# Optimization experiments

Measured on AMD Instinct MI355X. Metric: run time of the kernel, lower is better.

## Reference

```python
import jax, jax.numpy as jnp
import numpy as np


def setup_inputs() -> dict:
    key = jax.random.key(0)
    k1, k2, k3, k4 = jax.random.split(key, 4)
    B, G, C, T = 4, 40, 13, 1024
    return {
        "x": jax.random.normal(k1, (B, G, C, T), dtype=jnp.float32),
        "query_w": jax.random.normal(k2, (C, C), dtype=jnp.float32),
        "key_w": jax.random.normal(k3, (C, C), dtype=jnp.float32),
        "value_w": jax.random.normal(k4, (C, C), dtype=jnp.float32),
    }


def reference(x, query_w, key_w, value_w):
    # x: [B, 40, 13, T] real -> rfft over time -> [B, 40, 13, F] complex
    x_fft = jnp.fft.rfft(x, axis=-1)
    cdt = x_fft.dtype
    wq = query_w.astype(cdt)  # [13,13] complex (zero imag), shared across the 40 groups
    wk = key_w.astype(cdt)
    wv = value_w.astype(cdt)
    xt = jnp.swapaxes(x_fft, -1, -2)  # [B, 40, F, 13]
    q = xt @ wq                       # [B, 40, F, 13]
    k = xt @ wk
    v = xt @ wv
    scores = jnp.abs(q @ jnp.swapaxes(k, -1, -2))     # [B, 40, F, F] real
    attn = jax.nn.softmax(scores, axis=-1).astype(cdt)
    out = (attn @ v)                                   # [B, 40, F, 13]
    out = jnp.swapaxes(out, -1, -2)                    # [B, 40, 13, F]
    return jnp.fft.irfft(out, axis=-1)                 # [B, 40, 13, 2*(F-1)]
```

## Files before the change

kernel.cpp:

```cpp
#include <hip/hip_runtime.h>
#include <math.h>

#define BDIM 4
#define GDIM 40
#define CDIM 13
#define TDIM 1024
#define FDIM 513
#define BG   (BDIM*GDIM)
#define NROW (BG*FDIM)
#define NCHUNK 9
#define TK 64
#define QW 64

typedef _Float16 half4 __attribute__((ext_vector_type(4)));
typedef _Float16 half8 __attribute__((ext_vector_type(8)));
typedef float    f32x4 __attribute__((ext_vector_type(4)));

#define MFMA16(a, b, c) __builtin_amdgcn_mfma_f32_16x16x16f16((a), (b), (c), 0, 0, 0)

__device__ __forceinline__ unsigned bitrev10(unsigned x) { return __brev(x) >> 22; }

#define IDX(i) ((i) + ((i) >> 5))

__global__ __launch_bounds__(256) void fft_fwd2(const float* __restrict__ x,
                                                float2* __restrict__ xf) {
    __shared__ float re[1056], im[1056];
    const int s2 = blockIdx.x;
    const int sigA = 2 * s2, sigB = sigA + 1;
    const float* x1 = x + (size_t)sigA * TDIM;
    const float* x2 = x1 + TDIM;
    for (int t = threadIdx.x; t < 1024; t += 256) {
        unsigned r = bitrev10(t);
        re[IDX(r)] = x1[t];
        im[IDX(r)] = x2[t];
    }
    __syncthreads();
    for (int s = 0; s < 10; s += 2) {
        const int h   = 1 << s;
        const int g   = threadIdx.x;
        const int grp = g >> s;
        const int pos = g & (h - 1);
        const int i0  = (grp << (s + 2)) + pos;
        const int j0 = IDX(i0), j1 = IDX(i0 + h), j2 = IDX(i0 + 2 * h), j3 = IDX(i0 + 3 * h);
        float w1s, w1c, w2s, w2c;
        __sincosf(-(float)M_PI * (float)pos / (float)h, &w1s, &w1c);
        __sincosf(-(float)M_PI * (float)pos / (float)(2 * h), &w2s, &w2c);
        float ar = re[j0], ai = im[j0], br = re[j1], bi = im[j1];
        float cr = re[j2], ci = im[j2], dr = re[j3], di = im[j3];
        float t1;
        t1 = w1c * br - w1s * bi; bi = w1c * bi + w1s * br; br = t1;
        t1 = w1c * dr - w1s * di; di = w1c * di + w1s * dr; dr = t1;
        float e0r = ar + br, e0i = ai + bi, e1r = ar - br, e1i = ai - bi;
        float f0r = cr + dr, f0i = ci + di, f1r = cr - dr, f1i = ci - di;
        t1 = w2c * f0r - w2s * f0i; f0i = w2c * f0i + w2s * f0r; f0r = t1;
        t1 = w2s * f1r + w2c * f1i; f1i = w2s * f1i - w2c * f1r; f1r = t1;
        re[j0] = e0r + f0r; im[j0] = e0i + f0i;
        re[j2] = e0r - f0r; im[j2] = e0i - f0i;
        re[j1] = e1r + f1r; im[j1] = e1i + f1i;
        re[j3] = e1r - f1r; im[j3] = e1i - f1i;
        __syncthreads();
    }
    for (int f = threadIdx.x; f < FDIM; f += 256) {
        int fr = (1024 - f) & 1023;
        float zr = re[IDX(f)], zi = im[IDX(f)];
        float wr = re[IDX(fr)], wi = im[IDX(fr)];
        xf[(size_t)sigA * FDIM + f] =
            make_float2(0.5f * (zr + wr), 0.5f * (zi - wi));
        xf[(size_t)sigB * FDIM + f] =
            make_float2(0.5f * (zi + wi), 0.5f * (wr - zr));
    }
}

__global__ __launch_bounds__(256) void qkv_kernel(const float2* __restrict__ xf,
                           const float* __restrict__ wq,
                           const float* __restrict__ wk,
                           const float* __restrict__ wv,
                           float2* __restrict__ q,
                           _Float16* __restrict__ KP,
                           _Float16* __restrict__ VT) {
    __shared__ float2   Xs[QW * CDIM];
    __shared__ float    Ws[3 * CDIM * CDIM];
    __shared__ _Float16 KPs[QW * 72];
    __shared__ _Float16 VTs[32 * 72];

    const int bg    = blockIdx.x % BG;
    const int ch    = blockIdx.x / BG;
    const int f0    = ch * QW;
    const int nrows = min(QW, FDIM - f0);
    const int tid   = threadIdx.x;
    const int nitems = nrows * CDIM;

    for (int idx = tid; idx < nitems; idx += 256) {
        int c   = idx / nrows;
        int row = idx - c * nrows;
        Xs[row * CDIM + c] = xf[((size_t)bg * CDIM + c) * FDIM + f0 + row];
    }
    for (int idx = tid; idx < 3 * 169; idx += 256)
        Ws[idx] = (idx < 169) ? wq[idx] : ((idx < 338) ? wk[idx - 169] : wv[idx - 338]);
    for (int z = tid; z < 6 * QW; z += 256) {
        int rr = z >> 6, jj = z & 63;
        int pc = (rr < 3) ? (13 + rr) : (29 + (rr - 3));
        VTs[pc * 72 + jj] = (_Float16)0.f;
    }
    __syncthreads();

    for (int item = tid; item < nitems; item += 256) {
        int row = item / CDIM;
        int i   = item - row * CDIM;
        const float2* xrow = &Xs[row * CDIM];
        float qr = 0, qi = 0, kr = 0, ki = 0, vr = 0, vi = 0;
#pragma unroll
        for (int c = 0; c < CDIM; ++c) {
            float2 xc = xrow[c];
            float a = Ws[c * CDIM + i];       qr += xc.x * a; qi += xc.y * a;
            float b = Ws[169 + c * CDIM + i]; kr += xc.x * b; ki += xc.y * b;
            float d = Ws[338 + c * CDIM + i]; vr += xc.x * d; vi += xc.y * d;
        }
        q[((size_t)bg * FDIM + f0) * CDIM + item] = make_float2(qr, qi);
        _Float16* kp = KPs + row * 72;
        _Float16 h0 = (_Float16)kr, h1 = (_Float16)ki;
        kp[i]      = h0;
        kp[13 + i] = h1;
        kp[32 + i] = (_Float16)(kr - (float)h0);
        kp[45 + i] = (_Float16)(ki - (float)h1);
        if (i == 12) {
            *(unsigned*)(kp + 26) = 0u; *(unsigned*)(kp + 28) = 0u; *(unsigned*)(kp + 30) = 0u;
            *(unsigned*)(kp + 58) = 0u; *(unsigned*)(kp + 60) = 0u; *(unsigned*)(kp + 62) = 0u;
        }
        VTs[i * 72 + row]        = (_Float16)vr;
        VTs[(16 + i) * 72 + row] = (_Float16)vi;
    }
    __syncthreads();

    _Float16* KPg = KP + ((size_t)bg * FDIM + f0) * 64;
    _Float16* VTg = VT + (size_t)bg * 2 * 16 * 520 + f0;
    if (nrows == QW) {
        for (int idx = tid; idx < QW * 8; idx += 256) {
            int row = idx >> 3, gg = idx & 7;
            *(half8*)(KPg + row * 64 + gg * 8) = *(const half8*)(KPs + row * 72 + gg * 8);
        }
        for (int idx = tid; idx < 32 * 8; idx += 256) {
            int pc = idx >> 3, j8 = idx & 7;
            *(half8*)(VTg + pc * 520 + j8 * 8) = *(const half8*)(VTs + pc * 72 + j8 * 8);
        }
    } else {
        for (int idx = tid; idx < nrows * 8; idx += 256) {
            int row = idx >> 3, gg = idx & 7;
            *(half8*)(KPg + row * 64 + gg * 8) = *(const half8*)(KPs + row * 72 + gg * 8);
        }
        if (tid < 32) VTg[tid * 520] = VTs[tid * 72];
    }
}

__global__ __launch_bounds__(256, 4) void attn_kernel(const float2* __restrict__ q,
                                                      const _Float16* __restrict__ KP,
                                                      const _Float16* __restrict__ VT,
                                                      float2* __restrict__ outspec) {
    __shared__ __align__(16) _Float16 Klds[TK * 64];
    __shared__ __align__(16) _Float16 VTlds[2 * 16 * 72];

    const int bg    = blockIdx.x % BG;
    const int chunk = blockIdx.x / BG;
    const int tid   = threadIdx.x;
    const int w     = tid >> 6;
    const int lane  = tid & 63;
    const int qlane = lane & 15;
    const int g     = lane >> 4;
    const int frow  = chunk * 64 + w * 16 + qlane;
    const bool writer = (frow < FDIM);
    const int f     = writer ? frow : (FDIM - 1);
    const size_t rowbase = ((size_t)bg * FDIM + f) * CDIM;

    half4 uh[2], ul[2], u2h[2], u2l[2];
#pragma unroll
    for (int c01 = 0; c01 < 2; ++c01) {
#pragma unroll
        for (int j = 0; j < 4; ++j) {
            int k = c01 * 16 + 4 * g + j;
            float a = 0.f, b = 0.f;
            if (k < CDIM) {
                float2 t = q[rowbase + k];          a = t.x;  b = t.y;
            } else if (k < 2 * CDIM) {
                float2 t = q[rowbase + (k - CDIM)]; a = -t.y; b = t.x;
            }
            _Float16 ah = (_Float16)a;
            uh[c01][j]  = ah;
            ul[c01][j]  = (_Float16)(a - (float)ah);
            _Float16 bh = (_Float16)b;
            u2h[c01][j] = bh;
            u2l[c01][j] = (_Float16)(b - (float)bh);
        }
    }

    f32x4 o_re = {0.f, 0.f, 0.f, 0.f};
    f32x4 o_im = {0.f, 0.f, 0.f, 0.f};
    float m = -INFINITY, l = 0.f;

    const _Float16* __restrict__ KPg = KP + (size_t)bg * FDIM * 64;
    const _Float16* __restrict__ VTg = VT + (size_t)bg * 2 * 16 * 520;

    for (int t0 = 0; t0 < FDIM; t0 += TK) {
        __syncthreads();
#pragma unroll
        for (int hh = 0; hh < 2; ++hh) {
            int gr  = tid + hh * 256;
            int krw = gr >> 3, gg = gr & 7;
            half8 val;
#pragma unroll
            for (int e = 0; e < 8; ++e) val[e] = (_Float16)0.f;
            int grow = t0 + krw;
            if (grow < FDIM)
                val = *(const half8*)(KPg + (size_t)grow * 64 + gg * 8);
            *(half8*)(Klds + krw * 64 + ((gg ^ (krw & 7)) << 3)) = val;
        }
        {
            int gk = tid & 7, cc = (tid >> 3) & 15, part = tid >> 7;
            int rb = t0 + gk * 8;
            half8 val;
#pragma unroll
            for (int e = 0; e < 8; ++e) val[e] = (_Float16)0.f;
            if (rb < FDIM) {
                val = *(const half8*)(VTg + ((size_t)(part * 16 + cc)) * 520 + rb);
                if (rb + 8 > FDIM) {
#pragma unroll
                    for (int e = 0; e < 8; ++e) if (rb + e >= FDIM) val[e] = (_Float16)0.f;
                }
            }
            *(half8*)(VTlds + (part * 16 + cc) * 72 + gk * 8) = val;
        }
        __syncthreads();

#pragma unroll
        for (int sub = 0; sub < 4; ++sub) {
            const int arow = sub * 16 + qlane;
            const int rx   = arow & 7;
            const _Float16* kr = Klds + arow * 64;
#define KFRAG(h) (*(const half4*)(kr + (((((h) >> 3)) ^ rx) << 3) + ((h) & 7)))
            half4 wh0 = KFRAG(4 * g);
            half4 wh1 = KFRAG(16 + 4 * g);
            half4 wl0 = KFRAG(32 + 4 * g);
            half4 wl1 = KFRAG(48 + 4 * g);
#undef KFRAG
            f32x4 sre = {0.f, 0.f, 0.f, 0.f};
            f32x4 sim = {0.f, 0.f, 0.f, 0.f};
            sre = MFMA16(wh0, uh[0], sre);
            sre = MFMA16(wh1, uh[1], sre);
            sre = MFMA16(wl0, uh[0], sre);
            sre = MFMA16(wl1, uh[1], sre);
            sre = MFMA16(wh0, ul[0], sre);
            sre = MFMA16(wh1, ul[1], sre);
            sre = MFMA16(wl0, ul[0], sre);
            sre = MFMA16(wl1, ul[1], sre);
            sim = MFMA16(wh0, u2h[0], sim);
            sim = MFMA16(wh1, u2h[1], sim);
            sim = MFMA16(wl0, u2h[0], sim);
            sim = MFMA16(wl1, u2h[1], sim);
            sim = MFMA16(wh0, u2l[0], sim);
            sim = MFMA16(wh1, u2l[1], sim);
            sim = MFMA16(wl0, u2l[0], sim);
            sim = MFMA16(wl1, u2l[1], sim);

            float s0 = sqrtf(fmaf(sre[0], sre[0], sim[0] * sim[0]));
            float s1 = sqrtf(fmaf(sre[1], sre[1], sim[1] * sim[1]));
            float s2 = sqrtf(fmaf(sre[2], sre[2], sim[2] * sim[2]));
            float s3 = sqrtf(fmaf(sre[3], sre[3], sim[3] * sim[3]));
            float tmax = fmaxf(fmaxf(s0, s1), fmaxf(s2, s3));
            tmax = fmaxf(tmax, __shfl_xor(tmax, 16));
            tmax = fmaxf(tmax, __shfl_xor(tmax, 32));
            float mnew  = fmaxf(m, tmax);
            float alpha = __expf(m - mnew);
            m = mnew;
            l *= alpha;
            o_re *= alpha;
            o_im *= alpha;
            float p0 = __expf(s0 - m);
            float p1 = __expf(s1 - m);
            float p2 = __expf(s2 - m);
            float p3 = __expf(s3 - m);
            l += (p0 + p1) + (p2 + p3);
            half4 pk;
            pk[0] = (_Float16)p0; pk[1] = (_Float16)p1;
            pk[2] = (_Float16)p2; pk[3] = (_Float16)p3;

            const int voff = sub * 16 + 4 * g;
            half4 vfr = *(const half4*)(VTlds + qlane * 72 + voff);
            half4 vfi = *(const half4*)(VTlds + (16 + qlane) * 72 + voff);
            o_re = MFMA16(vfr, pk, o_re);
            o_im = MFMA16(vfi, pk, o_im);
        }
    }

    l += __shfl_xor(l, 16);
    l += __shfl_xor(l, 32);
    if (writer) {
        float inv = 1.f / l;
#pragma unroll
        for (int j = 0; j < 4; ++j) {
            int c = 4 * g + j;
            if (c < CDIM)
                outspec[((size_t)(bg * CDIM + c)) * FDIM + frow] =
                    make_float2(o_re[j] * inv, o_im[j] * inv);
        }
    }
}

__global__ __launch_bounds__(256) void fft_inv2(const float2* __restrict__ spec,
                                                float* __restrict__ out) {
    __shared__ float re[1056], im[1056];
    const int s2 = blockIdx.x;
    const float2* Y1 = spec + (size_t)(2 * s2) * FDIM;
    const float2* Y2 = Y1 + FDIM;
    for (int t = threadIdx.x; t < 1024; t += 256) {
        float a, b, c, d;
        if (t <= 512) {
            float2 y1 = Y1[t], y2 = Y2[t];
            bool edge = (t == 0) | (t == 512);
            a = y1.x; b = edge ? 0.f : y1.y;
            c = y2.x; d = edge ? 0.f : y2.y;
        } else {
            float2 y1 = Y1[1024 - t], y2 = Y2[1024 - t];
            a = y1.x; b = -y1.y;
            c = y2.x; d = -y2.y;
        }
        unsigned r = bitrev10(t);
        re[IDX(r)] = a - d;
        im[IDX(r)] = b + c;
    }
    __syncthreads();
    for (int s = 0; s < 10; s += 2) {
        const int h   = 1 << s;
        const int g   = threadIdx.x;
        const int grp = g >> s;
        const int pos = g & (h - 1);
        const int i0  = (grp << (s + 2)) + pos;
        const int j0 = IDX(i0), j1 = IDX(i0 + h), j2 = IDX(i0 + 2 * h), j3 = IDX(i0 + 3 * h);
        float w1s, w1c, w2s, w2c;
        __sincosf((float)M_PI * (float)pos / (float)h, &w1s, &w1c);
        __sincosf((float)M_PI * (float)pos / (float)(2 * h), &w2s, &w2c);
        float ar = re[j0], ai = im[j0], br = re[j1], bi = im[j1];
        float cr = re[j2], ci = im[j2], dr = re[j3], di = im[j3];
        float t1;
        t1 = w1c * br - w1s * bi; bi = w1c * bi + w1s * br; br = t1;
        t1 = w1c * dr - w1s * di; di = w1c * di + w1s * dr; dr = t1;
        float e0r = ar + br, e0i = ai + bi, e1r = ar - br, e1i = ai - bi;
        float f0r = cr + dr, f0i = ci + di, f1r = cr - dr, f1i = ci - di;
        t1 = w2c * f0r - w2s * f0i; f0i = w2c * f0i + w2s * f0r; f0r = t1;
        t1 = -w2s * f1r - w2c * f1i; f1i = -w2s * f1i + w2c * f1r; f1r = t1;
        re[j0] = e0r + f0r; im[j0] = e0i + f0i;
        re[j2] = e0r - f0r; im[j2] = e0i - f0i;
        re[j1] = e1r + f1r; im[j1] = e1i + f1i;
        re[j3] = e1r - f1r; im[j3] = e1i - f1i;
        __syncthreads();
    }
    const float scale = 1.0f / 1024.0f;
    float* o1 = out + (size_t)(2 * s2) * TDIM;
    for (int t = threadIdx.x; t < 1024; t += 256) {
        o1[t]        = re[IDX(t)] * scale;
        o1[TDIM + t] = im[IDX(t)] * scale;
    }
}

extern "C" void kernel_launch(void* const* d_in, const int* in_sizes, int n_in,
                              void* d_out, int out_size, void* d_ws, size_t ws_size,
                              hipStream_t stream) {
    const float* x  = (const float*)d_in[0];
    const float* wq = (const float*)d_in[1];
    const float* wk = (const float*)d_in[2];
    const float* wv = (const float*)d_in[3];
    float* out = (float*)d_out;

    const size_t n = (size_t)NROW * CDIM;
    float2* xf = (float2*)d_ws;
    float2* q  = xf + n;
    _Float16* KP = (_Float16*)(q + n);
    _Float16* VT = KP + (size_t)NROW * 64;

    fft_fwd2<<<BG * CDIM / 2, 256, 0, stream>>>(x, xf);
    qkv_kernel<<<BG * NCHUNK, 256, 0, stream>>>(xf, wq, wk, wv, q, KP, VT);
    attn_kernel<<<BG * NCHUNK, 256, 0, stream>>>(q, KP, VT, xf );
    fft_inv2<<<BG * CDIM / 2, 256, 0, stream>>>(xf, out);
}
```

Before: 159.6 us.

## Process two query chunks per attention block to reuse K/V tiles

Each attention block now handles two 64-row query chunks instead of one, so every K and V tile staged in shared memory feeds twice as many MFMA score and output computations. The grid shrinks from 9 to 5 chunk-blocks per batch-group, which halves the global-to-LDS tile loads and the barriers per query row. In exchange the kernel holds twice the register state (query fragments, accumulators, softmax stats), which may reduce occupancy under the 4-block launch bound. The grid becomes 800 blocks, and the final pair carries a partly empty second chunk.

```diff
diff --git a/kernel.cpp b/kernel.cpp
--- a/kernel.cpp
+++ b/kernel.cpp
@@ -9,6 +9,7 @@
 #define BG   (BDIM*GDIM)
 #define NROW (BG*FDIM)
 #define NCHUNK 9
+#define NPAIR 5
 #define TK 64
 #define QW 64
 
@@ -160,41 +161,49 @@
     __shared__ __align__(16) _Float16 VTlds[2 * 16 * 72];
 
     const int bg    = blockIdx.x % BG;
-    const int chunk = blockIdx.x / BG;
+    const int pr    = blockIdx.x / BG;
     const int tid   = threadIdx.x;
     const int w     = tid >> 6;
     const int lane  = tid & 63;
     const int qlane = lane & 15;
     const int g     = lane >> 4;
-    const int frow  = chunk * 64 + w * 16 + qlane;
-    const bool writer = (frow < FDIM);
-    const int f     = writer ? frow : (FDIM - 1);
-    const size_t rowbase = ((size_t)bg * FDIM + f) * CDIM;
-
-    half4 uh[2], ul[2], u2h[2], u2l[2];
-#pragma unroll
-    for (int c01 = 0; c01 < 2; ++c01) {
-#pragma unroll
-        for (int j = 0; j < 4; ++j) {
-            int k = c01 * 16 + 4 * g + j;
-            float a = 0.f, b = 0.f;
-            if (k < CDIM) {
-                float2 t = q[rowbase + k];          a = t.x;  b = t.y;
-            } else if (k < 2 * CDIM) {
-                float2 t = q[rowbase + (k - CDIM)]; a = -t.y; b = t.x;
+
+    half4 uh[2][2], ul[2][2], u2h[2][2], u2l[2][2];
+    int   frow_s[2];
+#pragma unroll
+    for (int s = 0; s < 2; ++s) {
+        frow_s[s] = (2 * pr + s) * 64 + w * 16 + qlane;
+        const int f = (frow_s[s] < FDIM) ? frow_s[s] : (FDIM - 1);
+        const size_t rowbase = ((size_t)bg * FDIM + f) * CDIM;
+#pragma unroll
+        for (int c01 = 0; c01 < 2; ++c01) {
+#pragma unroll
+            for (int j = 0; j < 4; ++j) {
+                int k = c01 * 16 + 4 * g + j;
+                float a = 0.f, b = 0.f;
+                if (k < CDIM) {
+                    float2 t = q[rowbase + k];          a = t.x;  b = t.y;
+                } else if (k < 2 * CDIM) {
+                    float2 t = q[rowbase + (k - CDIM)]; a = -t.y; b = t.x;
+                }
+                _Float16 ah = (_Float16)a;
+                uh[s][c01][j]  = ah;
+                ul[s][c01][j]  = (_Float16)(a - (float)ah);
+                _Float16 bh = (_Float16)b;
+                u2h[s][c01][j] = bh;
+                u2l[s][c01][j] = (_Float16)(b - (float)bh);
             }
-            _Float16 ah = (_Float16)a;
-            uh[c01][j]  = ah;
-            ul[c01][j]  = (_Float16)(a - (float)ah);
-            _Float16 bh = (_Float16)b;
-            u2h[c01][j] = bh;
-            u2l[c01][j] = (_Float16)(b - (float)bh);
-        }
-    }
-
-    f32x4 o_re = {0.f, 0.f, 0.f, 0.f};
-    f32x4 o_im = {0.f, 0.f, 0.f, 0.f};
-    float m = -INFINITY, l = 0.f;
+        }
+    }
+
+    f32x4 o_re[2], o_im[2];
+    float m[2], l[2];
+#pragma unroll
+    for (int s = 0; s < 2; ++s) {
+        o_re[s] = (f32x4){0.f, 0.f, 0.f, 0.f};
+        o_im[s] = (f32x4){0.f, 0.f, 0.f, 0.f};
+        m[s] = -INFINITY; l[s] = 0.f;
+    }
 
     const _Float16* __restrict__ KPg = KP + (size_t)bg * FDIM * 64;
     const _Float16* __restrict__ VTg = VT + (size_t)bg * 2 * 16 * 520;
@@ -241,65 +250,72 @@
             half4 wl0 = KFRAG(32 + 4 * g);
             half4 wl1 = KFRAG(48 + 4 * g);
 #undef KFRAG
-            f32x4 sre = {0.f, 0.f, 0.f, 0.f};
-            f32x4 sim = {0.f, 0.f, 0.f, 0.f};
-            sre = MFMA16(wh0, uh[0], sre);
-            sre = MFMA16(wh1, uh[1], sre);
-            sre = MFMA16(wl0, uh[0], sre);
-            sre = MFMA16(wl1, uh[1], sre);
-            sre = MFMA16(wh0, ul[0], sre);
-            sre = MFMA16(wh1, ul[1], sre);
-            sre = MFMA16(wl0, ul[0], sre);
-            sre = MFMA16(wl1, ul[1], sre);
-            sim = MFMA16(wh0, u2h[0], sim);
-            sim = MFMA16(wh1, u2h[1], sim);
-            sim = MFMA16(wl0, u2h[0], sim);
-            sim = MFMA16(wl1, u2h[1], sim);
-            sim = MFMA16(wh0, u2l[0], sim);
-            sim = MFMA16(wh1, u2l[1], sim);
-            sim = MFMA16(wl0, u2l[0], sim);
-            sim = MFMA16(wl1, u2l[1], sim);
-
-            float s0 = sqrtf(fmaf(sre[0], sre[0], sim[0] * sim[0]));
-            float s1 = sqrtf(fmaf(sre[1], sre[1], sim[1] * sim[1]));
-            float s2 = sqrtf(fmaf(sre[2], sre[2], sim[2] * sim[2]));
-            float s3 = sqrtf(fmaf(sre[3], sre[3], sim[3] * sim[3]));
-            float tmax = fmaxf(fmaxf(s0, s1), fmaxf(s2, s3));
-            tmax = fmaxf(tmax, __shfl_xor(tmax, 16));
-            tmax = fmaxf(tmax, __shfl_xor(tmax, 32));
-            float mnew  = fmaxf(m, tmax);
-            float alpha = __expf(m - mnew);
-            m = mnew;
-            l *= alpha;
-            o_re *= alpha;
-            o_im *= alpha;
-            float p0 = __expf(s0 - m);
-            float p1 = __expf(s1 - m);
-            float p2 = __expf(s2 - m);
-            float p3 = __expf(s3 - m);
-            l += (p0 + p1) + (p2 + p3);
-            half4 pk;
-            pk[0] = (_Float16)p0; pk[1] = (_Float16)p1;
-            pk[2] = (_Float16)p2; pk[3] = (_Float16)p3;
-
             const int voff = sub * 16 + 4 * g;
             half4 vfr = *(const half4*)(VTlds + qlane * 72 + voff);
             half4 vfi = *(const half4*)(VTlds + (16 + qlane) * 72 + voff);
-            o_re = MFMA16(vfr, pk, o_re);
-            o_im = MFMA16(vfi, pk, o_im);
-        }
-    }
-
-    l += __shfl_xor(l, 16);
-    l += __shfl_xor(l, 32);
-    if (writer) {
-        float inv = 1.f / l;
-#pragma unroll
-        for (int j = 0; j < 4; ++j) {
-            int c = 4 * g + j;
-            if (c < CDIM)
-                outspec[((size_t)(bg * CDIM + c)) * FDIM + frow] =
-                    make_float2(o_re[j] * inv, o_im[j] * inv);
+
+#pragma unroll
+            for (int s = 0; s < 2; ++s) {
+                f32x4 sre = {0.f, 0.f, 0.f, 0.f};
+                f32x4 sim = {0.f, 0.f, 0.f, 0.f};
+                sre = MFMA16(wh0, uh[s][0], sre);
+                sre = MFMA16(wh1, uh[s][1], sre);
+                sre = MFMA16(wl0, uh[s][0], sre);
+                sre = MFMA16(wl1, uh[s][1], sre);
+                sre = MFMA16(wh0, ul[s][0], sre);
+                sre = MFMA16(wh1, ul[s][1], sre);
+                sre = MFMA16(wl0, ul[s][0], sre);
+                sre = MFMA16(wl1, ul[s][1], sre);
+                sim = MFMA16(wh0, u2h[s][0], sim);
+                sim = MFMA16(wh1, u2h[s][1], sim);
+                sim = MFMA16(wl0, u2h[s][0], sim);
+                sim = MFMA16(wl1, u2h[s][1], sim);
+                sim = MFMA16(wh0, u2l[s][0], sim);
+                sim = MFMA16(wh1, u2l[s][1], sim);
+                sim = MFMA16(wl0, u2l[s][0], sim);
+                sim = MFMA16(wl1, u2l[s][1], sim);
+
+                float s0 = sqrtf(fmaf(sre[0], sre[0], sim[0] * sim[0]));
+                float s1 = sqrtf(fmaf(sre[1], sre[1], sim[1] * sim[1]));
+                float s2 = sqrtf(fmaf(sre[2], sre[2], sim[2] * sim[2]));
+                float s3 = sqrtf(fmaf(sre[3], sre[3], sim[3] * sim[3]));
+                float tmax = fmaxf(fmaxf(s0, s1), fmaxf(s2, s3));
+                tmax = fmaxf(tmax, __shfl_xor(tmax, 16));
+                tmax = fmaxf(tmax, __shfl_xor(tmax, 32));
+                float mnew  = fmaxf(m[s], tmax);
+                float alpha = __expf(m[s] - mnew);
+                m[s] = mnew;
+                l[s] *= alpha;
+                o_re[s] *= alpha;
+                o_im[s] *= alpha;
+                float p0 = __expf(s0 - m[s]);
+                float p1 = __expf(s1 - m[s]);
+                float p2 = __expf(s2 - m[s]);
+                float p3 = __expf(s3 - m[s]);
+                l[s] += (p0 + p1) + (p2 + p3);
+                half4 pk;
+                pk[0] = (_Float16)p0; pk[1] = (_Float16)p1;
+                pk[2] = (_Float16)p2; pk[3] = (_Float16)p3;
+                o_re[s] = MFMA16(vfr, pk, o_re[s]);
+                o_im[s] = MFMA16(vfi, pk, o_im[s]);
+            }
+        }
+    }
+
+#pragma unroll
+    for (int s = 0; s < 2; ++s) {
+        float lt = l[s];
+        lt += __shfl_xor(lt, 16);
+        lt += __shfl_xor(lt, 32);
+        if (frow_s[s] < FDIM) {
+            float inv = 1.f / lt;
+#pragma unroll
+            for (int j = 0; j < 4; ++j) {
+                int c = 4 * g + j;
+                if (c < CDIM)
+                    outspec[((size_t)(bg * CDIM + c)) * FDIM + frow_s[s]] =
+                        make_float2(o_re[s][j] * inv, o_im[s][j] * inv);
+            }
         }
     }
 }
@@ -377,6 +393,6 @@
 
     fft_fwd2<<<BG * CDIM / 2, 256, 0, stream>>>(x, xf);
     qkv_kernel<<<BG * NCHUNK, 256, 0, stream>>>(xf, wq, wk, wv, q, KP, VT);
-    attn_kernel<<<BG * NCHUNK, 256, 0, stream>>>(q, KP, VT, xf );
+    attn_kernel<<<BG * NPAIR, 256, 0, stream>>>(q, KP, VT, xf );
     fft_inv2<<<BG * CDIM / 2, 256, 0, stream>>>(xf, out);
 }
```

Result: slower. 178.3 us (+11.7%).
